# Performance work log

Measured on AMD Instinct MI355X. Metric: run time of the kernel, lower is better.

## Reference

```python
import jax, jax.numpy as jnp
import numpy as np

PHI = 1.618033988749895  # golden ratio
LUT_SIZE = 4096
TWO_PI = 2.0 * float(np.pi)
_grid = np.arange(LUT_SIZE, dtype=np.float32) * (TWO_PI / LUT_SIZE)
SIN_TABLE = jnp.asarray(np.sin(_grid).astype(np.float32))
COS_TABLE = jnp.asarray(np.cos(_grid).astype(np.float32))


def lut_sin_cos(theta):
    """4096-entry sin/cos lookup table over [0, 2pi) with linear interpolation."""
    pos = theta * (LUT_SIZE / TWO_PI)
    i0 = jnp.floor(pos)
    frac = (pos - i0).astype(theta.dtype)
    idx0 = jnp.mod(i0.astype(jnp.int32), LUT_SIZE)
    idx1 = jnp.mod(idx0 + 1, LUT_SIZE)
    sin_v = SIN_TABLE[idx0] * (1.0 - frac) + SIN_TABLE[idx1] * frac
    cos_v = COS_TABLE[idx0] * (1.0 - frac) + COS_TABLE[idx1] * frac
    return sin_v, cos_v


def _forward(input_ids, emb, w_query, b_query, w_key, b_key, w_ctx, W_res, B_res, w_pr, w_pi, w_out):
    B, S = input_ids.shape
    D = emb.shape[1] // 2
    H, dh = w_query.shape
    e = emb[input_ids]                               # [B,S,2D]
    w_emb, b_emb = e[..., :D], e[..., D:]
    t_arr = jnp.arange(S, dtype=jnp.float32)

    # --- sequential euler-transform recurrence (the only truly serial part) ---
    def step(carry, xs):
        h_r, h_i = carry
        w_t, b_t, t = xs                             # [B,D],[B,D],scalar
        wl = 1.0 + jnp.abs(w_t)
        tp = t * PHI
        th_r = h_r / wl + b_t + tp
        th_i = h_i / wl + b_t + tp
        sr, cr = lut_sin_cos(th_r)
        si, ci = lut_sin_cos(th_i)
        nr = cr * ci - sr * si
        ni = cr * si + sr * ci
        return (nr, ni), nr + ni

    init = (jnp.zeros((B, D), dtype=emb.dtype), jnp.zeros((B, D), dtype=emb.dtype))
    xs = (jnp.swapaxes(w_emb, 0, 1), jnp.swapaxes(b_emb, 0, 1), t_arr)
    _, states = jax.lax.scan(step, init, xs)         # [S,B,D]
    states = jnp.swapaxes(states, 0, 1)              # [B,S,D] == cached_states

    # --- multi-head LUT sin/cos attention over strictly-previous cached states ---
    xp = states.reshape(B, S, H, dh)                 # per-head patches
    t_phi = t_arr * PHI                              # [S]
    th_q = xp / (1.0 + jnp.abs(w_query)) + b_query + t_phi[None, :, None, None]
    sq, cq = lut_sin_cos(th_q)
    q = jnp.concatenate([cq, sq], axis=-1)           # [B,S,H,2dh]
    th_k = xp / (1.0 + jnp.abs(w_key)) + b_key
    sk, ck = lut_sin_cos(th_k)
    k = jnp.concatenate([ck, sk], axis=-1)           # [B,S,H,2dh]
    scale = float(np.sqrt(2.0 * dh))
    scores = jnp.einsum('bthd,bshd->bhts', q, k) / scale
    mask = jnp.tril(jnp.ones((S, S), dtype=bool), k=-1)   # keys strictly before query
    scores = jnp.where(mask[None, None], scores, -1e30)
    weights = jax.nn.softmax(scores, axis=-1)
    context = jnp.einsum('bhts,bsd->btd', weights, states)   # heads summed
    has_ctx = (t_arr > 0).astype(states.dtype)[None, :, None]  # t=0 has no cache
    x = states + has_ctx * (context @ w_ctx.T)

    # --- resonant layer over num_neurons ---
    wl_res = 1.0 + jnp.abs(W_res)                    # [N,D]
    theta = x[:, :, None, :] / wl_res + B_res + t_phi[None, :, None, None]  # [B,S,N,D]
    s_t, c_t = lut_sin_cos(theta)
    cos_sum = c_t.sum(-1)                            # [B,S,N]
    sin_sum = s_t.sum(-1)
    x = x + jax.nn.silu(cos_sum @ w_pr.T + sin_sum @ w_pi.T)

    return x @ w_out.T                               # [B,S,V]


def setup_inputs() -> dict:
    key = jax.random.key(0)
    ks = jax.random.split(key, 12)
    B, S, V, D, H, N = 8, 512, 32000, 64, 4, 128
    dh = D // H
    return {
        'input_ids': jax.random.randint(ks[0], (B, S), 0, V),
        'emb': jax.random.normal(ks[1], (V, 2 * D), dtype=jnp.float32) * 0.02,
        'w_query': jax.random.normal(ks[2], (H, dh), dtype=jnp.float32) * 0.02,
        'b_query': jnp.zeros((H, dh), dtype=jnp.float32),
        'w_key': jax.random.normal(ks[3], (H, dh), dtype=jnp.float32) * 0.02,
        'b_key': jnp.zeros((H, dh), dtype=jnp.float32),
        'w_ctx': jax.random.normal(ks[4], (D, D), dtype=jnp.float32) * 0.02,
        'W_res': jax.random.normal(ks[5], (N, D), dtype=jnp.float32) * 0.02,
        'B_res': jnp.zeros((N, D), dtype=jnp.float32),
        'w_pr': jax.random.normal(ks[6], (D, N), dtype=jnp.float32) * 0.02,
        'w_pi': jax.random.normal(ks[7], (D, N), dtype=jnp.float32) * 0.02,
        'w_out': jax.random.normal(ks[8], (V, D), dtype=jnp.float32) * 0.02,
    }


def reference(input_ids, emb, w_query, b_query, w_key, b_key, w_ctx, W_res, B_res, w_pr, w_pi, w_out):
    return _forward(input_ids, emb, w_query, b_query, w_key, b_key, w_ctx, W_res, B_res, w_pr, w_pi, w_out)
```

## Files before the change

kernel.cpp:

```cpp
#include <hip/hip_runtime.h>
#include <hip/hip_bf16.h>
#include <math.h>

#define PHI_F     1.618033988749895f
#define LUT_N     4096
#define LUT_INV   651.8986469044033f
#define LUT_STEP  0.0015339807878856412f

#define B_  8
#define S_  512
#define D_  64
#define H_  4
#define DH_ 16
#define N_  128
#define V_  32000
#define R_  (B_ * S_)

typedef __attribute__((ext_vector_type(8))) short short8_t;
typedef __attribute__((ext_vector_type(4))) float f32x4;

__device__ __forceinline__ void lut2(const float2* __restrict__ sc,
                                     float th, float& s, float& c) {
    float pos = th * LUT_INV;
    float f0  = floorf(pos);
    float fr  = pos - f0;
    int   i0  = ((int)f0) & (LUT_N - 1);
    int   i1  = (i0 + 1) & (LUT_N - 1);
    float2 p0 = sc[i0];
    float2 p1 = sc[i1];
    float om  = 1.0f - fr;
    s = p0.x * om + p1.x * fr;
    c = p0.y * om + p1.y * fr;
}

__global__ void k_tables(float2* __restrict__ scT) {
    int i = blockIdx.x * blockDim.x + threadIdx.x;
    if (i < LUT_N) {
        float g = (float)i * LUT_STEP;
        scT[i] = make_float2((float)sin((double)g), (float)cos((double)g));
    }
}

__global__ __launch_bounds__(256) void k_fused0(
        const int* __restrict__ ids, const float* __restrict__ emb,
        const float* __restrict__ Wres, const float* __restrict__ Bres,
        const float* __restrict__ wpr, const float* __restrict__ wpi,
        const float* __restrict__ wout, const float2* __restrict__ scT,
        float* __restrict__ states, __hip_bfloat16* __restrict__ wb,
        float2* __restrict__ ibres, float2* __restrict__ wpT) {
    int blk = blockIdx.x;
    int tid = threadIdx.x;
    if (blk >= 8) {
        if (blk < 2008) {
            int i = (blk - 8) * 256 + tid;
            float4 v = ((const float4*)wout)[i];
            union { __hip_bfloat16 h[4]; short4 s4; } u;
            u.h[0] = __float2bfloat16(v.x);
            u.h[1] = __float2bfloat16(v.y);
            u.h[2] = __float2bfloat16(v.z);
            u.h[3] = __float2bfloat16(v.w);
            *(short4*)(&wb[4 * (size_t)i]) = u.s4;
        } else {
            int idx = (blk - 2008) * 256 + tid;
            ibres[idx] = make_float2(1.0f / (1.0f + fabsf(Wres[idx])), Bres[idx]);
            int nn = idx >> 6, d = idx & 63;
            wpT[idx] = make_float2(wpr[d * N_ + nn], wpi[d * N_ + nn]);
        }
        return;
    }
    __shared__ float2 sc[LUT_N];
    __shared__ int idsh[S_];
    for (int i = tid; i < LUT_N; i += 256) sc[i] = scT[i];
    for (int i = tid; i < S_; i += 256) idsh[i] = ids[blk * S_ + i];
    __syncthreads();
    if (tid >= 64) return;
    int d = tid, b = blk;
    float cw[8], cb[8], nw[8], nb[8];
#pragma unroll
    for (int j = 0; j < 8; ++j) {
        int id = idsh[j];
        cw[j] = emb[(size_t)id * 128 + d];
        cb[j] = emb[(size_t)id * 128 + 64 + d];
    }
    float* outp = states + (size_t)b * S_ * D_ + d;
    float hr = 0.0f, hi = 0.0f;
    for (int tc = 0; tc < S_; tc += 8) {
#pragma unroll
        for (int jj = 0; jj < 8; ++jj) {
            int id = idsh[(tc + 8 + jj) & (S_ - 1)];
            nw[jj] = emb[(size_t)id * 128 + d];
            nb[jj] = emb[(size_t)id * 128 + 64 + d];
        }
#pragma unroll
        for (int jj = 0; jj < 8; ++jj) {
            int   t   = tc + jj;
            float wl  = 1.0f + fabsf(cw[jj]);
            float btv = cb[jj];
            float tp  = (float)t * PHI_F;
            float thr = hr / wl + btv + tp;
            float thi = hi / wl + btv + tp;
            float sr, cr, si, ci;
            lut2(sc, thr, sr, cr);
            lut2(sc, thi, si, ci);
            float nr = cr * ci - sr * si;
            float ni = cr * si + sr * ci;
            hr = nr; hi = ni;
            outp[t * D_] = nr + ni;
        }
#pragma unroll
        for (int jj = 0; jj < 8; ++jj) { cw[jj] = nw[jj]; cb[jj] = nb[jj]; }
    }
}

__global__ __launch_bounds__(256) void k_qk(const float* __restrict__ states,
                                            const float* __restrict__ wq,
                                            const float* __restrict__ bq,
                                            const float* __restrict__ wk,
                                            const float* __restrict__ bk,
                                            const float2* __restrict__ scT,
                                            float* __restrict__ q,
                                            float* __restrict__ kT) {
    __shared__ float2 sc[LUT_N];
    for (int i = threadIdx.x; i < LUT_N; i += 256) sc[i] = scT[i];
    __syncthreads();
    const int total = R_ * H_ * DH_;
    for (int idx = blockIdx.x * 256 + threadIdx.x; idx < total; idx += gridDim.x * 256) {
        int j  = idx & (DH_ - 1);
        int h  = (idx >> 4) & (H_ - 1);
        int bt = idx >> 6;
        int t  = bt & (S_ - 1);
        int b  = bt >> 9;
        float xp = states[idx];
        float tp = (float)t * PHI_F;
        int   hj = h * DH_ + j;
        float thq = xp / (1.0f + fabsf(wq[hj])) + bq[hj] + tp;
        float thk = xp / (1.0f + fabsf(wk[hj])) + bk[hj];
        float sq, cq, sk, ck;
        lut2(sc, thq, sq, cq);
        lut2(sc, thk, sk, ck);
        int base = bt * (H_ * 2 * DH_) + h * (2 * DH_) + j;
        q[base] = cq; q[base + DH_] = sq;
        size_t kb = ((size_t)(b * H_ + h) * 32 + j) * S_ + t;
        kT[kb] = ck; kT[kb + 16 * S_] = sk;
    }
}

__global__ __launch_bounds__(256) void k_attn(const float* __restrict__ states,
                                              const float* __restrict__ q,
                                              const float* __restrict__ kT,
                                              const float* __restrict__ wctx,
                                              float* __restrict__ x) {
    int bt = blockIdx.x;
    int b  = bt >> 9, t = bt & (S_ - 1);
    int tid = threadIdx.x;
    if (t == 0) {
        if (tid < D_) x[bt * D_ + tid] = states[bt * D_ + tid];
        return;
    }
    __shared__ float wlds[H_][S_];
    __shared__ float ql[H_][2 * DH_];
    __shared__ float cpart[4][D_];
    int h = tid >> 6, l = tid & 63;
    if (l < 2 * DH_) ql[h][l] = q[bt * 128 + h * 32 + l];
    __syncthreads();

    const float* kTb = kT + (size_t)(b * H_ + h) * 32 * S_;
    float sc[8];
    float m = -INFINITY;
#pragma unroll
    for (int jj = 0; jj < 8; ++jj) {
        int s = l + jj * 64;
        float v = -INFINITY;
        if (s < t) {
            float acc = 0.0f;
#pragma unroll
            for (int c = 0; c < 32; ++c)
                acc = fmaf(kTb[c * S_ + s], ql[h][c], acc);
            v = acc * 0.1767766952966369f;
            m = fmaxf(m, v);
        }
        sc[jj] = v;
    }
    for (int o = 32; o; o >>= 1) m = fmaxf(m, __shfl_xor(m, o));
    float sum = 0.0f;
#pragma unroll
    for (int jj = 0; jj < 8; ++jj) {
        float e = __expf(sc[jj] - m);
        sc[jj] = e; sum += e;
    }
    for (int o = 32; o; o >>= 1) sum += __shfl_xor(sum, o);
    float inv = 1.0f / sum;
#pragma unroll
    for (int jj = 0; jj < 8; ++jj) {
        int s = l + jj * 64;
        if (s < S_) wlds[h][s] = sc[jj] * inv;
    }
    __syncthreads();
    {
        int dd = tid & 63, p = tid >> 6;
        float acc = 0.0f;
        for (int s = p; s < t; s += 4) {
            float w4 = wlds[0][s] + wlds[1][s] + wlds[2][s] + wlds[3][s];
            acc += w4 * states[((size_t)b * S_ + s) * D_ + dd];
        }
        cpart[p][dd] = acc;
    }
    __syncthreads();
    if (tid < D_) {
        float c = cpart[0][tid] + cpart[1][tid] + cpart[2][tid] + cpart[3][tid];
        cpart[0][tid] = c;
    }
    __syncthreads();
    if (tid < D_) {
        float y = 0.0f;
        const float* wr = wctx + tid * D_;
        for (int dd = 0; dd < D_; ++dd) y += cpart[0][dd] * wr[dd];
        x[bt * D_ + tid] = states[bt * D_ + tid] + y;
    }
}

__global__ __launch_bounds__(256) void k_resid(const float* __restrict__ x,
                                               const float2* __restrict__ ibres,
                                               const float2* __restrict__ wpT,
                                               const float2* __restrict__ scT,
                                               __hip_bfloat16* __restrict__ xb) {
    __shared__ float2 sc[LUT_N];
    __shared__ float xv[D_];
    __shared__ float csum[N_], ssum[N_];
    __shared__ float part[4][D_];
    int tid = threadIdx.x;
    for (int i = tid; i < LUT_N; i += 256) sc[i] = scT[i];
    int n  = tid >> 1;
    int d0 = (tid & 1) * 32;
    float2 ib[32];
#pragma unroll
    for (int dd = 0; dd < 32; ++dd) ib[dd] = ibres[n * D_ + d0 + dd];
    int g = tid >> 6, dl = tid & 63;
    for (int r = 0; r < 8; ++r) {
        int bt = blockIdx.x * 8 + r;
        int t  = bt & (S_ - 1);
        float tp = (float)t * PHI_F;
        __syncthreads();
        if (tid < D_) xv[tid] = x[bt * D_ + tid];
        __syncthreads();
        float cs = 0.0f, ss = 0.0f;
#pragma unroll
        for (int dd = 0; dd < 32; ++dd) {
            float th = fmaf(xv[d0 + dd], ib[dd].x, ib[dd].y) + tp;
            float s, c;
            lut2(sc, th, s, c);
            cs += c; ss += s;
        }
        cs += __shfl_xor(cs, 1);
        ss += __shfl_xor(ss, 1);
        if ((tid & 1) == 0) { csum[n] = cs; ssum[n] = ss; }
        __syncthreads();
        float acc = 0.0f;
#pragma unroll
        for (int nn = 0; nn < 32; ++nn) {
            float2 w = wpT[(g * 32 + nn) * D_ + dl];
            acc = fmaf(csum[g * 32 + nn], w.x, fmaf(ssum[g * 32 + nn], w.y, acc));
        }
        part[g][dl] = acc;
        __syncthreads();
        if (tid < D_) {
            float pre = part[0][tid] + part[1][tid] + part[2][tid] + part[3][tid];
            float sig = 1.0f / (1.0f + __expf(-pre));
            xb[bt * D_ + tid] = __float2bfloat16(xv[tid] + pre * sig);
        }
    }
}

__global__ __launch_bounds__(256) void k_out(const __hip_bfloat16* __restrict__ xb,
                                             const __hip_bfloat16* __restrict__ wb,
                                             float* __restrict__ out) {
    __shared__ float ot[64][132];
    int tid  = threadIdx.x;
    int wave = tid >> 6, l = tid & 63;
    int wr = wave >> 1, wc = wave & 1;
    int m0 = blockIdx.y * 64 + wr * 32;
    int r  = l & 15;
    int ks = (l >> 4) * 8;
    int kh = l >> 4;

    short8_t a[2][2];
#pragma unroll
    for (int mi = 0; mi < 2; ++mi)
#pragma unroll
        for (int kk = 0; kk < 2; ++kk)
            a[mi][kk] = *reinterpret_cast<const short8_t*>(
                xb + (size_t)(m0 + mi * 16 + r) * 64 + kk * 32 + ks);

    for (int ch = 0; ch < 2; ++ch) {
        int c0 = blockIdx.x * 256 + ch * 128 + wc * 64;
        short8_t b[4][2];
#pragma unroll
        for (int ni = 0; ni < 4; ++ni)
#pragma unroll
            for (int kk = 0; kk < 2; ++kk)
                b[ni][kk] = *reinterpret_cast<const short8_t*>(
                    wb + (size_t)(c0 + ni * 16 + r) * 64 + kk * 32 + ks);

        f32x4 acc[2][4];
#pragma unroll
        for (int mi = 0; mi < 2; ++mi)
#pragma unroll
            for (int ni = 0; ni < 4; ++ni) {
                acc[mi][ni] = (f32x4){0.f, 0.f, 0.f, 0.f};
                acc[mi][ni] = __builtin_amdgcn_mfma_f32_16x16x32_bf16(
                    a[mi][0], b[ni][0], acc[mi][ni], 0, 0, 0);
                acc[mi][ni] = __builtin_amdgcn_mfma_f32_16x16x32_bf16(
                    a[mi][1], b[ni][1], acc[mi][ni], 0, 0, 0);
            }

        if (ch) __syncthreads();
#pragma unroll
        for (int mi = 0; mi < 2; ++mi)
#pragma unroll
            for (int ni = 0; ni < 4; ++ni)
#pragma unroll
                for (int i = 0; i < 4; ++i)
                    ot[wr * 32 + mi * 16 + kh * 4 + i][wc * 64 + ni * 16 + r] = acc[mi][ni][i];
        __syncthreads();

        size_t rbase = blockIdx.y * 64;
        size_t cb    = (size_t)blockIdx.x * 256 + ch * 128;
#pragma unroll
        for (int j = 0; j < 8; ++j) {
            int idx = j * 256 + tid;
            int row = idx >> 5, c4 = idx & 31;
            float4 v = *(const float4*)&ot[row][c4 * 4];
            *(float4*)&out[(rbase + row) * V_ + cb + c4 * 4] = v;
        }
    }
}

extern "C" void kernel_launch(void* const* d_in, const int* in_sizes, int n_in,
                              void* d_out, int out_size, void* d_ws, size_t ws_size,
                              hipStream_t stream) {
    const int*   ids  = (const int*)  d_in[0];
    const float* emb  = (const float*)d_in[1];
    const float* wq   = (const float*)d_in[2];
    const float* bq   = (const float*)d_in[3];
    const float* wk   = (const float*)d_in[4];
    const float* bk   = (const float*)d_in[5];
    const float* wctx = (const float*)d_in[6];
    const float* Wres = (const float*)d_in[7];
    const float* Bres = (const float*)d_in[8];
    const float* wpr  = (const float*)d_in[9];
    const float* wpi  = (const float*)d_in[10];
    const float* wout = (const float*)d_in[11];
    float* out = (float*)d_out;

    float* states = (float*)d_ws;
    float* qbuf   = states + R_ * D_;
    float* kTbuf  = qbuf + R_ * 128;
    float* xbuf   = kTbuf + B_ * H_ * 32 * S_;
    __hip_bfloat16* wb = (__hip_bfloat16*)(xbuf + R_ * D_);
    __hip_bfloat16* xb = wb + (size_t)V_ * D_;
    float2* scT   = (float2*)(xb + R_ * D_);
    float2* ibres = scT + LUT_N;
    float2* wpT   = ibres + N_ * D_;

    k_tables<<<16, 256, 0, stream>>>(scT);
    k_fused0<<<2040, 256, 0, stream>>>(ids, emb, Wres, Bres, wpr, wpi, wout, scT,
                                       states, wb, ibres, wpT);
    k_qk    <<<64, 256, 0, stream>>>(states, wq, bq, wk, bk, scT, qbuf, kTbuf);
    k_attn  <<<R_, 256, 0, stream>>>(states, qbuf, kTbuf, wctx, xbuf);
    k_resid <<<R_ / 8, 256, 0, stream>>>(xbuf, ibres, wpT, scT, xb);
    k_out   <<<dim3(V_ / 256, R_ / 64), 256, 0, stream>>>(xb, wb, out);
}
```

Measured before the change: 353.8 us.

## Tile attention over four query rows per block and widen qk grid

The attention kernel now processes four consecutive query positions per block. Each key column is loaded once and reused for four dot products, and each states row is reused for four context accumulations. This cuts redundant global reads and the launch count from 4096 blocks to 1024. The qk kernel becomes one element per thread across 1024 blocks instead of a grid-stride loop over 64 blocks, which raises parallelism but repeats the LUT staging into shared memory per block. The output GEMM store becomes a nontemporal store to avoid polluting the cache with the large logits tensor.

```diff
diff --git a/kernel.cpp b/kernel.cpp
--- a/kernel.cpp
+++ b/kernel.cpp
@@ -123,8 +123,8 @@
     __shared__ float2 sc[LUT_N];
     for (int i = threadIdx.x; i < LUT_N; i += 256) sc[i] = scT[i];
     __syncthreads();
-    const int total = R_ * H_ * DH_;
-    for (int idx = blockIdx.x * 256 + threadIdx.x; idx < total; idx += gridDim.x * 256) {
+    {
+        int idx = blockIdx.x * 256 + threadIdx.x;
         int j  = idx & (DH_ - 1);
         int h  = (idx >> 4) & (H_ - 1);
         int bt = idx >> 6;
@@ -145,77 +145,114 @@
     }
 }
 
+#define TB_ 4
 __global__ __launch_bounds__(256) void k_attn(const float* __restrict__ states,
                                               const float* __restrict__ q,
                                               const float* __restrict__ kT,
                                               const float* __restrict__ wctx,
                                               float* __restrict__ x) {
-    int bt = blockIdx.x;
-    int b  = bt >> 9, t = bt & (S_ - 1);
+    __shared__ float ql[H_][TB_][2 * DH_];
+    __shared__ float wlds[H_][TB_][S_];
+    __shared__ float cpart[4][TB_][D_];
+    __shared__ float ctx[TB_][D_];
+    int blk = blockIdx.x;
+    int b = blk >> 7, tile = blk & 127;
+    int t0 = tile * TB_;
     int tid = threadIdx.x;
-    if (t == 0) {
-        if (tid < D_) x[bt * D_ + tid] = states[bt * D_ + tid];
-        return;
-    }
-    __shared__ float wlds[H_][S_];
-    __shared__ float ql[H_][2 * DH_];
-    __shared__ float cpart[4][D_];
     int h = tid >> 6, l = tid & 63;
-    if (l < 2 * DH_) ql[h][l] = q[bt * 128 + h * 32 + l];
+    if (l < 2 * DH_) {
+#pragma unroll
+        for (int tt = 0; tt < TB_; ++tt)
+            ql[h][tt][l] = q[((b << 9) + t0 + tt) * 128 + h * 32 + l];
+    }
     __syncthreads();
 
     const float* kTb = kT + (size_t)(b * H_ + h) * 32 * S_;
-    float sc[8];
-    float m = -INFINITY;
+    float sc[8][TB_];
+    float m[TB_];
+#pragma unroll
+    for (int tt = 0; tt < TB_; ++tt) m[tt] = -INFINITY;
 #pragma unroll
     for (int jj = 0; jj < 8; ++jj) {
         int s = l + jj * 64;
-        float v = -INFINITY;
-        if (s < t) {
-            float acc = 0.0f;
-#pragma unroll
-            for (int c = 0; c < 32; ++c)
-                acc = fmaf(kTb[c * S_ + s], ql[h][c], acc);
-            v = acc * 0.1767766952966369f;
-            m = fmaxf(m, v);
-        }
-        sc[jj] = v;
-    }
-    for (int o = 32; o; o >>= 1) m = fmaxf(m, __shfl_xor(m, o));
-    float sum = 0.0f;
-#pragma unroll
-    for (int jj = 0; jj < 8; ++jj) {
-        float e = __expf(sc[jj] - m);
-        sc[jj] = e; sum += e;
-    }
-    for (int o = 32; o; o >>= 1) sum += __shfl_xor(sum, o);
-    float inv = 1.0f / sum;
-#pragma unroll
-    for (int jj = 0; jj < 8; ++jj) {
-        int s = l + jj * 64;
-        if (s < S_) wlds[h][s] = sc[jj] * inv;
+        float a0 = 0.f, a1 = 0.f, a2 = 0.f, a3 = 0.f;
+        if (s < t0 + TB_ - 1) {
+#pragma unroll
+            for (int c = 0; c < 32; ++c) {
+                float kv = kTb[c * S_ + s];
+                a0 = fmaf(kv, ql[h][0][c], a0);
+                a1 = fmaf(kv, ql[h][1][c], a1);
+                a2 = fmaf(kv, ql[h][2][c], a2);
+                a3 = fmaf(kv, ql[h][3][c], a3);
+            }
+        }
+        const float scale = 0.1767766952966369f;
+        float v0 = (s < t0 + 0) ? a0 * scale : -INFINITY;
+        float v1 = (s < t0 + 1) ? a1 * scale : -INFINITY;
+        float v2 = (s < t0 + 2) ? a2 * scale : -INFINITY;
+        float v3 = (s < t0 + 3) ? a3 * scale : -INFINITY;
+        sc[jj][0] = v0; m[0] = fmaxf(m[0], v0);
+        sc[jj][1] = v1; m[1] = fmaxf(m[1], v1);
+        sc[jj][2] = v2; m[2] = fmaxf(m[2], v2);
+        sc[jj][3] = v3; m[3] = fmaxf(m[3], v3);
+    }
+#pragma unroll
+    for (int tt = 0; tt < TB_; ++tt)
+        for (int o = 32; o; o >>= 1) m[tt] = fmaxf(m[tt], __shfl_xor(m[tt], o));
+    float sum[TB_] = {0.f, 0.f, 0.f, 0.f};
+#pragma unroll
+    for (int jj = 0; jj < 8; ++jj)
+#pragma unroll
+        for (int tt = 0; tt < TB_; ++tt) {
+            float e = __expf(sc[jj][tt] - m[tt]);
+            sc[jj][tt] = e; sum[tt] += e;
+        }
+#pragma unroll
+    for (int tt = 0; tt < TB_; ++tt)
+        for (int o = 32; o; o >>= 1) sum[tt] += __shfl_xor(sum[tt], o);
+#pragma unroll
+    for (int tt = 0; tt < TB_; ++tt) {
+        float inv = 1.0f / sum[tt];
+#pragma unroll
+        for (int jj = 0; jj < 8; ++jj)
+            wlds[h][tt][l + jj * 64] = sc[jj][tt] * inv;
     }
     __syncthreads();
     {
-        int dd = tid & 63, p = tid >> 6;
-        float acc = 0.0f;
-        for (int s = p; s < t; s += 4) {
-            float w4 = wlds[0][s] + wlds[1][s] + wlds[2][s] + wlds[3][s];
-            acc += w4 * states[((size_t)b * S_ + s) * D_ + dd];
-        }
-        cpart[p][dd] = acc;
-    }
-    __syncthreads();
-    if (tid < D_) {
-        float c = cpart[0][tid] + cpart[1][tid] + cpart[2][tid] + cpart[3][tid];
-        cpart[0][tid] = c;
-    }
-    __syncthreads();
-    if (tid < D_) {
-        float y = 0.0f;
-        const float* wr = wctx + tid * D_;
-        for (int dd = 0; dd < D_; ++dd) y += cpart[0][dd] * wr[dd];
-        x[bt * D_ + tid] = states[bt * D_ + tid] + y;
+        int p = tid >> 6, d = tid & 63;
+        float ac[TB_] = {0.f, 0.f, 0.f, 0.f};
+        for (int s = p; s < t0 + TB_ - 1; s += 4) {
+            float sv = states[(((size_t)b << 9) + s) * D_ + d];
+#pragma unroll
+            for (int tt = 0; tt < TB_; ++tt) {
+                float w4 = wlds[0][tt][s] + wlds[1][tt][s]
+                         + wlds[2][tt][s] + wlds[3][tt][s];
+                if (s < t0 + tt) ac[tt] += w4 * sv;
+            }
+        }
+#pragma unroll
+        for (int tt = 0; tt < TB_; ++tt) cpart[p][tt][d] = ac[tt];
+    }
+    __syncthreads();
+    {
+        int tt = tid >> 6, dd = tid & 63;
+        ctx[tt][dd] = cpart[0][tt][dd] + cpart[1][tt][dd]
+                    + cpart[2][tt][dd] + cpart[3][tt][dd];
+    }
+    __syncthreads();
+    {
+        int tt = tid >> 6, dd = tid & 63;
+        int t  = t0 + tt;
+        size_t row = ((size_t)b << 9) + t;
+        float base = states[row * D_ + dd];
+        float val  = base;
+        if (t > 0) {
+            float y = 0.0f;
+            const float* wr = wctx + dd * D_;
+            for (int k = 0; k < D_; ++k) y += ctx[tt][k] * wr[k];
+            val = base + y;
+        }
+        x[row * D_ + dd] = val;
     }
 }
 
@@ -329,8 +366,9 @@
         for (int j = 0; j < 8; ++j) {
             int idx = j * 256 + tid;
             int row = idx >> 5, c4 = idx & 31;
-            float4 v = *(const float4*)&ot[row][c4 * 4];
-            *(float4*)&out[(rbase + row) * V_ + cb + c4 * 4] = v;
+            f32x4 v = *(const f32x4*)&ot[row][c4 * 4];
+            __builtin_nontemporal_store(v,
+                (f32x4*)&out[(rbase + row) * V_ + cb + c4 * 4]);
         }
     }
 }
@@ -365,8 +403,8 @@
     k_tables<<<16, 256, 0, stream>>>(scT);
     k_fused0<<<2040, 256, 0, stream>>>(ids, emb, Wres, Bres, wpr, wpi, wout, scT,
                                        states, wb, ibres, wpT);
-    k_qk    <<<64, 256, 0, stream>>>(states, wq, bq, wk, bk, scT, qbuf, kTbuf);
-    k_attn  <<<R_, 256, 0, stream>>>(states, qbuf, kTbuf, wctx, xbuf);
+    k_qk    <<<1024, 256, 0, stream>>>(states, wq, bq, wk, bk, scT, qbuf, kTbuf);
+    k_attn  <<<1024, 256, 0, stream>>>(states, qbuf, kTbuf, wctx, xbuf);
     k_resid <<<R_ / 8, 256, 0, stream>>>(xbuf, ibres, wpT, scT, xb);
     k_out   <<<dim3(V_ / 256, R_ / 64), 256, 0, stream>>>(xb, wb, out);
 }
```

New measurement: 326.0 us. -7.9%, faster.
